# Performance work log

Measured on AMD Instinct MI355X. Metric: run time of the kernel, lower is better.

The kernel has to match this reference:

```python
import jax, jax.numpy as jnp
import numpy as np
import math

B, S, D = 4, 2048, 1024
H = 16
HD = D // H  # 64
NEG_INF = -1e9


def setup_inputs() -> dict:
    key = jax.random.key(0)
    k1, k2, k3, k4, k5 = jax.random.split(key, 5)
    x = jax.random.normal(k1, (B, S, D), dtype=jnp.float32)
    # rotary frequencies (theta = 10000), shape (S, HD//2)
    inv_freq = 1.0 / (10000.0 ** (jnp.arange(0, HD, 2, dtype=jnp.float32) / HD))
    t = jnp.arange(S, dtype=jnp.float32)
    freqs = jnp.outer(t, inv_freq)  # (S, HD//2)
    freqs_cos = jnp.cos(freqs)
    freqs_sin = jnp.sin(freqs)
    # causal additive mask (1,1,S,S)
    causal = jnp.tril(jnp.ones((S, S), dtype=bool))
    mask = jnp.where(causal, 0.0, NEG_INF).astype(jnp.float32)[None, None]
    scale = 0.02
    wq = jax.random.normal(k2, (D, D), dtype=jnp.float32) * scale
    wk = jax.random.normal(k3, (D, D), dtype=jnp.float32) * scale
    wv = jax.random.normal(k4, (D, D), dtype=jnp.float32) * scale
    wo = jax.random.normal(k5, (D, D), dtype=jnp.float32) * scale
    return {"x": x, "freqs_cos": freqs_cos, "freqs_sin": freqs_sin,
            "mask": mask, "wq": wq, "wk": wk, "wv": wv, "wo": wo}


def _apply_rotary(t, cos, sin):
    # t: (B,S,H,HD); cos/sin: (S, HD//2) broadcast as (1,S,1,HD//2)
    tr = t.reshape(*t.shape[:-1], HD // 2, 2)
    t0, t1 = tr[..., 0], tr[..., 1]
    c = cos[None, :, None, :]
    s = sin[None, :, None, :]
    o0 = t0 * c - t1 * s
    o1 = t0 * s + t1 * c
    return jnp.stack([o0, o1], axis=-1).reshape(t.shape)


def reference(x, freqs_cos, freqs_sin, mask, wq, wk, wv, wo):
    bsz, seqlen, _ = x.shape
    xq = (x @ wq).reshape(bsz, seqlen, H, HD)
    xk = (x @ wk).reshape(bsz, seqlen, H, HD)
    xv = (x @ wv).reshape(bsz, seqlen, H, HD)
    xq = _apply_rotary(xq, freqs_cos, freqs_sin)
    xk = _apply_rotary(xk, freqs_cos, freqs_sin)
    # (B,H,S,HD)
    xq = xq.transpose(0, 2, 1, 3)
    xk = xk.transpose(0, 2, 1, 3)
    xv = xv.transpose(0, 2, 1, 3)
    scores = jnp.einsum('bhqd,bhkd->bhqk', xq, xk) / math.sqrt(HD)
    scores = scores + mask
    probs = jax.nn.softmax(scores.astype(jnp.float32), axis=-1).astype(xq.dtype)
    # dropout is identity in eval mode
    out = jnp.einsum('bhqk,bhkd->bhqd', probs, xv)
    out = out.transpose(0, 2, 1, 3).reshape(bsz, seqlen, H * HD)
    return out @ wo
```

## Files before the change

### kernel.cpp

```cpp
#include <hip/hip_runtime.h>
#include <stdint.h>

typedef short short8 __attribute__((ext_vector_type(8)));
typedef float f32x4 __attribute__((ext_vector_type(4)));
typedef float f32x16 __attribute__((ext_vector_type(16)));
typedef unsigned int u32x4 __attribute__((ext_vector_type(4)));
typedef float float4e __attribute__((ext_vector_type(4)));
typedef unsigned short u16;

#define BB 4
#define SS 2048
#define DD 1024
#define HH 16
#define MM (BB*SS)

__device__ __forceinline__ u16 f2bf(float f) {
    unsigned u = __float_as_uint(f);
    u += 0x7FFFu + ((u >> 16) & 1u);
    return (u16)(u >> 16);
}
__device__ __forceinline__ float bf2f(u16 h) {
    return __uint_as_float(((unsigned)h) << 16);
}
__device__ __forceinline__ unsigned cvtpk(float a, float b) {
    unsigned r;
    asm("v_cvt_pk_bf16_f32 %0, %1, %2" : "=v"(r) : "v"(a), "v"(b));
    return r;
}
__device__ __forceinline__ void gload16(const void* g, void* l) {
    __builtin_amdgcn_global_load_lds(
        (const __attribute__((address_space(1))) unsigned int*)(uintptr_t)g,
        (__attribute__((address_space(3))) unsigned int*)(unsigned)(uintptr_t)l,
        16, 0, 0);
}
__device__ __forceinline__ bool tens_is_bf(const u16* mref) { return mref[1] == 0xCE6Eu; }

__global__ __launch_bounds__(256) void cvt_x(const void* xin, u16* xb, const u16* mref) {
    bool isbf = tens_is_bf(mref);
    size_t i = (size_t)blockIdx.x * 256 + threadIdx.x;
    if (isbf) {
        ((u32x4*)xb)[i] = ((const u32x4*)xin)[i];
    } else {
        const float4e* src = (const float4e*)xin;
        float4e a = src[2*i], b = src[2*i+1];
        u32x4 o;
        o[0] = (unsigned)f2bf(a[0]) | ((unsigned)f2bf(a[1]) << 16);
        o[1] = (unsigned)f2bf(a[2]) | ((unsigned)f2bf(a[3]) << 16);
        o[2] = (unsigned)f2bf(b[0]) | ((unsigned)f2bf(b[1]) << 16);
        o[3] = (unsigned)f2bf(b[2]) | ((unsigned)f2bf(b[3]) << 16);
        ((u32x4*)xb)[i] = o;
    }
}

__global__ __launch_bounds__(256) void trw(const void* w0, const void* w1, const void* w2, const void* w3,
                                           u16* wt, const u16* mref) {
    bool isbf = tens_is_bf(mref);
    const void* w = (blockIdx.z == 0) ? w0 : (blockIdx.z == 1) ? w1 : (blockIdx.z == 2) ? w2 : w3;
    u16* out = wt + (size_t)blockIdx.z * (DD*DD);
    __shared__ float t[32][33];
    int tx = threadIdx.x & 31, ty = threadIdx.x >> 5;
    int n0 = blockIdx.x * 32, k0 = blockIdx.y * 32;
#pragma unroll
    for (int i = 0; i < 4; ++i) {
        int k = k0 + ty*4 + i;
        float v = isbf ? bf2f(((const u16*)w)[(size_t)k*DD + n0 + tx])
                       : ((const float*)w)[(size_t)k*DD + n0 + tx];
        t[ty*4 + i][tx] = v;
    }
    __syncthreads();
#pragma unroll
    for (int i = 0; i < 4; ++i)
        out[(size_t)(n0 + ty*4 + i)*DD + k0 + tx] = f2bf(t[tx][ty*4 + i]);
}

template<int MODE>
__global__ __launch_bounds__(256) void gemm128(const u16* __restrict__ A, const u16* __restrict__ Bt,
                                               void* Cout, const void* fcos, const void* fsin,
                                               const u16* mref, float oscale) {
    constexpr int SMEMB = (MODE == 2) ? 36864 : 32768;
    __shared__ __align__(16) unsigned char smem[SMEMB];
    int tid = threadIdx.x;
    int w = tid >> 6, l = tid & 63, lo = l & 15, hi = l >> 4;
    int wm = w >> 1, wn = w & 1;
    int m0 = blockIdx.x * 128, n0 = blockIdx.y * 128;

    f32x4 acc[4][4] = {};

    auto stage = [&](int buf, int t) {
        int k0 = t * 32;
#pragma unroll
        for (int i = 0; i < 2; ++i) {
            int o = (i*256 + tid) * 16;
            int row = o >> 6, inb = o & 63;
            int sw  = inb ^ ((row & 3) << 4);
            gload16((const char*)A + ((size_t)(m0 + row)*DD + k0)*2 + sw,
                    smem + buf*16384 + (i*256 + (tid & ~63))*16);
            gload16((const char*)Bt + ((size_t)(n0 + row)*DD + k0)*2 + sw,
                    smem + buf*16384 + 8192 + (i*256 + (tid & ~63))*16);
        }
    };

    stage(0, 0);
    __syncthreads();
    int cur = 0;
    const int NT = DD / 32;
    for (int t = 0; t < NT; ++t) {
        if (t + 1 < NT) stage(cur ^ 1, t + 1);
        const char* Ab = (const char*)(smem + cur*16384);
        const char* Bb = Ab + 8192;
        short8 af[4], bfr[4];
#pragma unroll
        for (int mi = 0; mi < 4; ++mi) {
            int r = wm*64 + mi*16 + lo;
            int ib = hi * 16;
            af[mi] = *(const short8*)(Ab + r*64 + (ib ^ ((r & 3) << 4)));
        }
#pragma unroll
        for (int ni = 0; ni < 4; ++ni) {
            int r = wn*64 + ni*16 + lo;
            int ib = hi * 16;
            bfr[ni] = *(const short8*)(Bb + r*64 + (ib ^ ((r & 3) << 4)));
        }
        __builtin_amdgcn_s_setprio(1);
#pragma unroll
        for (int mi = 0; mi < 4; ++mi)
#pragma unroll
            for (int ni = 0; ni < 4; ++ni)
                acc[mi][ni] = __builtin_amdgcn_mfma_f32_16x16x32_bf16(af[mi], bfr[ni], acc[mi][ni], 0, 0, 0);
        __builtin_amdgcn_s_setprio(0);
        __syncthreads();
        cur ^= 1;
    }

    if (MODE == 0) {
        bool fbf = (((const u16*)fcos)[0] == 0x3F80u);
        u16* outp = (u16*)Cout;
#pragma unroll
        for (int mi = 0; mi < 4; ++mi)
#pragma unroll
            for (int ni = 0; ni < 4; ++ni)
#pragma unroll
                for (int r = 0; r < 4; ++r) {
                    int gm = m0 + wm*64 + mi*16 + hi*4 + r;
                    int gc = n0 + wn*64 + ni*16 + lo;
                    float v  = acc[mi][ni][r];
                    float vp = __shfl_xor(v, 1);
                    int s = gm & (SS-1), d = gc & 63, i2 = d >> 1;
                    float c, sn;
                    if (fbf) { c = bf2f(((const u16*)fcos)[s*32 + i2]); sn = bf2f(((const u16*)fsin)[s*32 + i2]); }
                    else     { c = ((const float*)fcos)[s*32 + i2];     sn = ((const float*)fsin)[s*32 + i2]; }
                    float o = (gc & 1) ? (vp*sn + v*c) : (v*c - vp*sn);
                    o *= oscale;
                    int b = gm >> 11, h = gc >> 6;
                    outp[((((size_t)b*HH + h)*SS + s) << 6) + d] = f2bf(o);
                }
    } else if (MODE == 2) {
        __syncthreads();
        u16* vs = (u16*)smem + w * (64*72);
#pragma unroll
        for (int ni = 0; ni < 4; ++ni) {
            int d = ni*16 + lo;
#pragma unroll
            for (int mi = 0; mi < 4; ++mi)
#pragma unroll
                for (int rr = 0; rr < 2; ++rr) {
                    unsigned pk = (unsigned)f2bf(acc[mi][ni][2*rr]) | ((unsigned)f2bf(acc[mi][ni][2*rr+1]) << 16);
                    *(unsigned*)(vs + d*72 + mi*16 + hi*4 + rr*2) = pk;
                }
        }
        asm volatile("s_waitcnt lgkmcnt(0)" ::: "memory");
        int bq = (m0 + wm*64) >> 11;
        int s_base = (m0 + wm*64) & (SS-1);
        int h = (n0 + wn*64) >> 6;
        u16* outp = (u16*)Cout;
#pragma unroll
        for (int p = 0; p < 8; ++p) {
            int idx = p*64 + l;
            int row = idx >> 3, ch = idx & 7;
            short8 vv = *(const short8*)(vs + row*72 + ch*8);
            *(short8*)(outp + (((size_t)bq*HH + h)*64 + row)*SS + s_base + ch*8) = vv;
        }
    } else {
        bool isbf = tens_is_bf(mref);
#pragma unroll
        for (int mi = 0; mi < 4; ++mi)
#pragma unroll
            for (int ni = 0; ni < 4; ++ni)
#pragma unroll
                for (int r = 0; r < 4; ++r) {
                    int gm = m0 + wm*64 + mi*16 + hi*4 + r;
                    int gc = n0 + wn*64 + ni*16 + lo;
                    float v = acc[mi][ni][r];
                    if (isbf) ((u16*)Cout)[(size_t)gm*DD + gc] = f2bf(v);
                    else      ((float*)Cout)[(size_t)gm*DD + gc] = v;
                }
    }
}

__global__ __launch_bounds__(256) void attn(const u16* __restrict__ Q, const u16* __restrict__ K,
                                            const u16* __restrict__ VT, u16* __restrict__ AO) {
    __shared__ __align__(16) u16 Kl[2][64*64];
    __shared__ __align__(16) u16 Vl[2][64*64];
    int bh = blockIdx.x;
    int qt = (gridDim.y - 1) - blockIdx.y;
    int tid = threadIdx.x, w = tid >> 6, l = tid & 63;
    int l31 = l & 31, hi5 = l >> 5;
    const u16* Qb = Q  + (size_t)bh * SS * 64;
    const u16* Kb = K  + (size_t)bh * SS * 64;
    const u16* Vb = VT + (size_t)bh * 64 * SS;
    int q0w = qt*128 + w*32;
    int q   = q0w + l31;

    short8 qf[4];
#pragma unroll
    for (int kc = 0; kc < 4; ++kc)
        qf[kc] = *(const short8*)(Qb + (size_t)q*64 + kc*16 + hi5*8);

    f32x16 oacc[2] = {};
    float m_ = -1e30f, l_ = 0.f;

    auto stage = [&](int buf, int kt) {
        const char* Kt = (const char*)(Kb + (size_t)kt*64*64);
        const char* Vt = (const char*)Vb + (size_t)kt*128;
#pragma unroll
        for (int i = 0; i < 2; ++i) {
            int idx = i*256 + tid;
            int row = idx >> 3, inb = (idx & 7) * 16;
            int sw = inb ^ ((row & 7) << 4);
            gload16(Kt + row*128 + sw,            (char*)Kl[buf] + (i*256 + (tid & ~63))*16);
            gload16(Vt + (size_t)row*(SS*2) + sw, (char*)Vl[buf] + (i*256 + (tid & ~63))*16);
        }
    };

    int nkt = 2*qt + 2;
    stage(0, 0);
    __syncthreads();
    int cur = 0;

    for (int kt = 0; kt < nkt; ++kt) {
        if (kt + 1 < nkt) stage(cur ^ 1, kt + 1);

        if (kt*64 <= q0w + 31) {
            f32x16 sc[2] = {};
            __builtin_amdgcn_s_setprio(1);
#pragma unroll
            for (int kvt = 0; kvt < 2; ++kvt) {
                short8 kf[4];
#pragma unroll
                for (int kc = 0; kc < 4; ++kc) {
                    int row = kvt*32 + l31;
                    int ib = kc*32 + hi5*16;
                    kf[kc] = *(const short8*)((const char*)Kl[cur] + row*128 + (ib ^ ((row & 7) << 4)));
                }
#pragma unroll
                for (int kc = 0; kc < 4; ++kc)
                    sc[kvt] = __builtin_amdgcn_mfma_f32_32x32x16_bf16(kf[kc], qf[kc], sc[kvt], 0, 0, 0);
            }
            __builtin_amdgcn_s_setprio(0);

            if (kt*64 + 63 > q0w) {
#pragma unroll
                for (int kvt = 0; kvt < 2; ++kvt)
#pragma unroll
                    for (int rg = 0; rg < 16; ++rg) {
                        int kv = kt*64 + kvt*32 + (rg & 3) + 8*(rg >> 2) + 4*hi5;
                        if (kv > q) sc[kvt][rg] = -1e9f;
                    }
            }

            float mx = -1e30f;
#pragma unroll
            for (int kvt = 0; kvt < 2; ++kvt)
#pragma unroll
                for (int rg = 0; rg < 16; ++rg) mx = fmaxf(mx, sc[kvt][rg]);
            mx = fmaxf(mx, __shfl_xor(mx, 32));
            float mn = fmaxf(m_, mx);
            float al = __expf(m_ - mn);
            float rs = 0.f;
#pragma unroll
            for (int kvt = 0; kvt < 2; ++kvt)
#pragma unroll
                for (int rg = 0; rg < 16; ++rg) {
                    float p = __expf(sc[kvt][rg] - mn);
                    sc[kvt][rg] = p;
                    rs += p;
                }
            rs += __shfl_xor(rs, 32);
            m_ = mn;
            l_ = l_ * al + rs;
#pragma unroll
            for (int dt = 0; dt < 2; ++dt)
#pragma unroll
                for (int rg = 0; rg < 16; ++rg) oacc[dt][rg] *= al;

            short8 pa[4];
#pragma unroll
            for (int kc = 0; kc < 4; ++kc) {
                const int kvt = kc >> 1;
                const int base = (kc & 1) * 8;
                unsigned A0 = cvtpk(sc[kvt][base + 0], sc[kvt][base + 1]);
                unsigned A1 = cvtpk(sc[kvt][base + 2], sc[kvt][base + 3]);
                unsigned B0 = cvtpk(sc[kvt][base + 4], sc[kvt][base + 5]);
                unsigned B1 = cvtpk(sc[kvt][base + 6], sc[kvt][base + 7]);
                asm("v_permlane32_swap_b32 %0, %1" : "+v"(A0), "+v"(B0));
                asm("v_permlane32_swap_b32 %0, %1" : "+v"(A1), "+v"(B1));
                u32x4 pk; pk[0] = A0; pk[1] = A1; pk[2] = B0; pk[3] = B1;
                pa[kc] = __builtin_bit_cast(short8, pk);
            }

            __builtin_amdgcn_s_setprio(1);
#pragma unroll
            for (int dt = 0; dt < 2; ++dt) {
                short8 vf[4];
#pragma unroll
                for (int kc = 0; kc < 4; ++kc) {
                    int row = dt*32 + l31;
                    int ib = kc*32 + hi5*16;
                    vf[kc] = *(const short8*)((const char*)Vl[cur] + row*128 + (ib ^ ((row & 7) << 4)));
                }
#pragma unroll
                for (int kc = 0; kc < 4; ++kc)
                    oacc[dt] = __builtin_amdgcn_mfma_f32_32x32x16_bf16(vf[kc], pa[kc], oacc[dt], 0, 0, 0);
            }
            __builtin_amdgcn_s_setprio(0);
        }

        __syncthreads();
        cur ^= 1;
    }

    int b = bh >> 4, h = bh & 15;
    float inv = 1.0f / l_;
    u16* aor = AO + (size_t)(b*SS + q)*DD + h*64;
#pragma unroll
    for (int dt = 0; dt < 2; ++dt)
#pragma unroll
        for (int j = 0; j < 8; ++j) {
            int r0 = 2*j, r1 = 2*j + 1;
            int d = dt*32 + (r0 & 3) + 8*(r0 >> 2) + 4*hi5;
            unsigned pk = (unsigned)f2bf(oacc[dt][r0] * inv) | ((unsigned)f2bf(oacc[dt][r1] * inv) << 16);
            *(unsigned*)(aor + d) = pk;
        }
}

extern "C" void kernel_launch(void* const* d_in, const int* in_sizes, int n_in,
                              void* d_out, int out_size, void* d_ws, size_t ws_size,
                              hipStream_t stream) {
    const void* x    = d_in[0];
    const void* fcos = d_in[1];
    const void* fsin = d_in[2];
    const u16*  mref = (const u16*)d_in[3];
    const void* wq   = d_in[4];
    const void* wk   = d_in[5];
    const void* wv   = d_in[6];
    const void* wo   = d_in[7];

    u16* ws = (u16*)d_ws;
    const size_t XB = (size_t)MM * DD;
    const size_t WT = (size_t)DD * DD;
    u16* xb  = ws;
    u16* wt  = ws + XB;
    u16* qb  = ws + XB + 4*WT;
    u16* kb  = qb + XB;
    u16* vtb = kb + XB;

    cvt_x<<<4096, 256, 0, stream>>>(x, xb, mref);
    trw<<<dim3(32, 32, 4), 256, 0, stream>>>(wq, wk, wv, wo, wt, mref);
    gemm128<0><<<dim3(64, 8), 256, 0, stream>>>(xb, wt,        qb,  fcos, fsin, mref, 0.125f);
    gemm128<0><<<dim3(64, 8), 256, 0, stream>>>(xb, wt + WT,   kb,  fcos, fsin, mref, 1.0f);
    gemm128<2><<<dim3(64, 8), 256, 0, stream>>>(xb, wt + 2*WT, vtb, fcos, fsin, mref, 1.0f);
    attn<<<dim3(64, 16), 256, 0, stream>>>(qb, kb, vtb, xb);
    gemm128<3><<<dim3(64, 8), 256, 0, stream>>>(xb, wt + 3*WT, d_out, fcos, fsin, mref, 1.0f);
}
```

Baseline: 194.8 us.

## Fuse QKV projections into one launch, add grid swizzle and lazy softmax rescale

The three Q/K/V projection GEMMs now run as a single 1536-block launch over the concatenated transposed weights, and each tile picks the Q, K or V-transpose epilogue from its column range. Block indices are remapped so groups of consecutive workgroups share weight tiles, which should improve L2 reuse. In attention, the Q scale now folds in log2(e) so the softmax can use exp2f, and the running-max rescale of the accumulators is skipped unless the new max exceeds the old one by more than 8. The intent is to cut launch overhead, tail effects and softmax VALU work. The lazy rescale lets unnormalised exponentials reach up to 2^8, which assumes fp32 and bf16 headroom is enough.

```diff
diff --git a/kernel.cpp b/kernel.cpp
--- a/kernel.cpp
+++ b/kernel.cpp
@@ -73,16 +73,22 @@
         out[(size_t)(n0 + ty*4 + i)*DD + k0 + tx] = f2bf(t[tx][ty*4 + i]);
 }
 
+#define QSCALE 0.1803368801111204f
 template<int MODE>
 __global__ __launch_bounds__(256) void gemm128(const u16* __restrict__ A, const u16* __restrict__ Bt,
-                                               void* Cout, const void* fcos, const void* fsin,
-                                               const u16* mref, float oscale) {
-    constexpr int SMEMB = (MODE == 2) ? 36864 : 32768;
+                                               u16* outQ, u16* outK, u16* outVT, void* Cout,
+                                               const void* fcos, const void* fsin,
+                                               const u16* mref) {
+    constexpr int SMEMB = (MODE == 1) ? 36864 : 32768;
     __shared__ __align__(16) unsigned char smem[SMEMB];
     int tid = threadIdx.x;
     int w = tid >> 6, l = tid & 63, lo = l & 15, hi = l >> 4;
     int wm = w >> 1, wn = w & 1;
-    int m0 = blockIdx.x * 128, n0 = blockIdx.y * 128;
+    int wg = blockIdx.x;
+    int c = wg & 7, local = wg >> 3;
+    int bx = c*8 + (local & 7);
+    int by = local >> 3;
+    int m0 = bx * 128, n0 = by * 128;
 
     f32x4 acc[4][4] = {};
 
@@ -132,53 +138,57 @@
         cur ^= 1;
     }
 
-    if (MODE == 0) {
-        bool fbf = (((const u16*)fcos)[0] == 0x3F80u);
-        u16* outp = (u16*)Cout;
-#pragma unroll
-        for (int mi = 0; mi < 4; ++mi)
-#pragma unroll
-            for (int ni = 0; ni < 4; ++ni)
-#pragma unroll
-                for (int r = 0; r < 4; ++r) {
-                    int gm = m0 + wm*64 + mi*16 + hi*4 + r;
-                    int gc = n0 + wn*64 + ni*16 + lo;
-                    float v  = acc[mi][ni][r];
-                    float vp = __shfl_xor(v, 1);
-                    int s = gm & (SS-1), d = gc & 63, i2 = d >> 1;
-                    float c, sn;
-                    if (fbf) { c = bf2f(((const u16*)fcos)[s*32 + i2]); sn = bf2f(((const u16*)fsin)[s*32 + i2]); }
-                    else     { c = ((const float*)fcos)[s*32 + i2];     sn = ((const float*)fsin)[s*32 + i2]; }
-                    float o = (gc & 1) ? (vp*sn + v*c) : (v*c - vp*sn);
-                    o *= oscale;
-                    int b = gm >> 11, h = gc >> 6;
-                    outp[((((size_t)b*HH + h)*SS + s) << 6) + d] = f2bf(o);
-                }
-    } else if (MODE == 2) {
-        __syncthreads();
-        u16* vs = (u16*)smem + w * (64*72);
-#pragma unroll
-        for (int ni = 0; ni < 4; ++ni) {
-            int d = ni*16 + lo;
+    if (MODE == 1) {
+        int wi = n0 >> 10;
+        int n0w = n0 & 1023;
+        if (wi == 2) {
+            __syncthreads();
+            u16* vs = (u16*)smem + w * (64*72);
+#pragma unroll
+            for (int ni = 0; ni < 4; ++ni) {
+                int d = ni*16 + lo;
+#pragma unroll
+                for (int mi = 0; mi < 4; ++mi)
+#pragma unroll
+                    for (int rr = 0; rr < 2; ++rr) {
+                        unsigned pk = (unsigned)f2bf(acc[mi][ni][2*rr]) | ((unsigned)f2bf(acc[mi][ni][2*rr+1]) << 16);
+                        *(unsigned*)(vs + d*72 + mi*16 + hi*4 + rr*2) = pk;
+                    }
+            }
+            asm volatile("s_waitcnt lgkmcnt(0)" ::: "memory");
+            int bq = (m0 + wm*64) >> 11;
+            int s_base = (m0 + wm*64) & (SS-1);
+            int h = (n0w + wn*64) >> 6;
+#pragma unroll
+            for (int p = 0; p < 8; ++p) {
+                int idx = p*64 + l;
+                int row = idx >> 3, ch = idx & 7;
+                short8 vv = *(const short8*)(vs + row*72 + ch*8);
+                *(short8*)(outVT + (((size_t)bq*HH + h)*64 + row)*SS + s_base + ch*8) = vv;
+            }
+        } else {
+            bool fbf = (((const u16*)fcos)[0] == 0x3F80u);
+            u16* outp = wi ? outK : outQ;
+            float oscale = wi ? 1.0f : QSCALE;
 #pragma unroll
             for (int mi = 0; mi < 4; ++mi)
 #pragma unroll
-                for (int rr = 0; rr < 2; ++rr) {
-                    unsigned pk = (unsigned)f2bf(acc[mi][ni][2*rr]) | ((unsigned)f2bf(acc[mi][ni][2*rr+1]) << 16);
-                    *(unsigned*)(vs + d*72 + mi*16 + hi*4 + rr*2) = pk;
-                }
-        }
-        asm volatile("s_waitcnt lgkmcnt(0)" ::: "memory");
-        int bq = (m0 + wm*64) >> 11;
-        int s_base = (m0 + wm*64) & (SS-1);
-        int h = (n0 + wn*64) >> 6;
-        u16* outp = (u16*)Cout;
-#pragma unroll
-        for (int p = 0; p < 8; ++p) {
-            int idx = p*64 + l;
-            int row = idx >> 3, ch = idx & 7;
-            short8 vv = *(const short8*)(vs + row*72 + ch*8);
-            *(short8*)(outp + (((size_t)bq*HH + h)*64 + row)*SS + s_base + ch*8) = vv;
+                for (int ni = 0; ni < 4; ++ni)
+#pragma unroll
+                    for (int r = 0; r < 4; ++r) {
+                        int gm = m0 + wm*64 + mi*16 + hi*4 + r;
+                        int gc = n0w + wn*64 + ni*16 + lo;
+                        float v  = acc[mi][ni][r];
+                        float vp = __shfl_xor(v, 1);
+                        int s = gm & (SS-1), d = gc & 63, i2 = d >> 1;
+                        float co, sn;
+                        if (fbf) { co = bf2f(((const u16*)fcos)[s*32 + i2]); sn = bf2f(((const u16*)fsin)[s*32 + i2]); }
+                        else     { co = ((const float*)fcos)[s*32 + i2];     sn = ((const float*)fsin)[s*32 + i2]; }
+                        float o = (gc & 1) ? (vp*sn + v*co) : (v*co - vp*sn);
+                        o *= oscale;
+                        int b = gm >> 11, h = gc >> 6;
+                        outp[((((size_t)b*HH + h)*SS + s) << 6) + d] = f2bf(o);
+                    }
         }
     } else {
         bool isbf = tens_is_bf(mref);
@@ -274,24 +284,27 @@
 #pragma unroll
                 for (int rg = 0; rg < 16; ++rg) mx = fmaxf(mx, sc[kvt][rg]);
             mx = fmaxf(mx, __shfl_xor(mx, 32));
-            float mn = fmaxf(m_, mx);
-            float al = __expf(m_ - mn);
+            if (!__all(mx <= m_ + 8.f)) {
+                float mn = fmaxf(m_, mx);
+                float al = exp2f(m_ - mn);
+                m_ = mn;
+                l_ *= al;
+#pragma unroll
+                for (int dt = 0; dt < 2; ++dt)
+#pragma unroll
+                    for (int rg = 0; rg < 16; ++rg) oacc[dt][rg] *= al;
+            }
             float rs = 0.f;
 #pragma unroll
             for (int kvt = 0; kvt < 2; ++kvt)
 #pragma unroll
                 for (int rg = 0; rg < 16; ++rg) {
-                    float p = __expf(sc[kvt][rg] - mn);
+                    float p = exp2f(sc[kvt][rg] - m_);
                     sc[kvt][rg] = p;
                     rs += p;
                 }
             rs += __shfl_xor(rs, 32);
-            m_ = mn;
-            l_ = l_ * al + rs;
-#pragma unroll
-            for (int dt = 0; dt < 2; ++dt)
-#pragma unroll
-                for (int rg = 0; rg < 16; ++rg) oacc[dt][rg] *= al;
+            l_ += rs;
 
             short8 pa[4];
 #pragma unroll
@@ -366,9 +379,7 @@
 
     cvt_x<<<4096, 256, 0, stream>>>(x, xb, mref);
     trw<<<dim3(32, 32, 4), 256, 0, stream>>>(wq, wk, wv, wo, wt, mref);
-    gemm128<0><<<dim3(64, 8), 256, 0, stream>>>(xb, wt,        qb,  fcos, fsin, mref, 0.125f);
-    gemm128<0><<<dim3(64, 8), 256, 0, stream>>>(xb, wt + WT,   kb,  fcos, fsin, mref, 1.0f);
-    gemm128<2><<<dim3(64, 8), 256, 0, stream>>>(xb, wt + 2*WT, vtb, fcos, fsin, mref, 1.0f);
+    gemm128<1><<<1536, 256, 0, stream>>>(xb, wt, qb, kb, vtb, nullptr, fcos, fsin, mref);
     attn<<<dim3(64, 16), 256, 0, stream>>>(qb, kb, vtb, xb);
-    gemm128<3><<<dim3(64, 8), 256, 0, stream>>>(xb, wt + 3*WT, d_out, fcos, fsin, mref, 1.0f);
-}
+    gemm128<3><<<512, 256, 0, stream>>>(xb, wt + 3*WT, nullptr, nullptr, nullptr, d_out, fcos, fsin, mref);
+}
```

New measurement: 200.5 us. 2.9% more time.

## Triple-buffer attention K/V loads and use exp2 softmax with lazy rescaling

Applied to the files above, without the earlier changes.

The attention kernel moves from double to triple buffering of the K/V LDS tiles. It prefetches two tiles ahead and replaces __syncthreads with explicit vmcnt waits plus a raw barrier. Softmax now works in base 2: log2(e)/sqrt(d) is folded into the Q scale, __expf becomes exp2f, and the running-max rescale of the output accumulator only happens when the new max exceeds the old one by more than 8. Swizzled LDS offsets are hoisted out of the loop, and the max and sum reductions are tree-structured. The cost is more LDS per block, which may reduce occupancy, and the vmcnt counting must stay correct.

```diff
diff --git a/kernel.cpp b/kernel.cpp
--- a/kernel.cpp
+++ b/kernel.cpp
@@ -34,6 +34,7 @@
         16, 0, 0);
 }
 __device__ __forceinline__ bool tens_is_bf(const u16* mref) { return mref[1] == 0xCE6Eu; }
+#define PIPE_BAR() do { __builtin_amdgcn_sched_barrier(0); __builtin_amdgcn_s_barrier(); __builtin_amdgcn_sched_barrier(0); } while(0)
 
 __global__ __launch_bounds__(256) void cvt_x(const void* xin, u16* xb, const u16* mref) {
     bool isbf = tens_is_bf(mref);
@@ -73,6 +74,7 @@
         out[(size_t)(n0 + ty*4 + i)*DD + k0 + tx] = f2bf(t[tx][ty*4 + i]);
 }
 
+#define QSCALE 0.1803368801111204f
 template<int MODE>
 __global__ __launch_bounds__(256) void gemm128(const u16* __restrict__ A, const u16* __restrict__ Bt,
                                                void* Cout, const void* fcos, const void* fsin,
@@ -146,10 +148,10 @@
                     float v  = acc[mi][ni][r];
                     float vp = __shfl_xor(v, 1);
                     int s = gm & (SS-1), d = gc & 63, i2 = d >> 1;
-                    float c, sn;
-                    if (fbf) { c = bf2f(((const u16*)fcos)[s*32 + i2]); sn = bf2f(((const u16*)fsin)[s*32 + i2]); }
-                    else     { c = ((const float*)fcos)[s*32 + i2];     sn = ((const float*)fsin)[s*32 + i2]; }
-                    float o = (gc & 1) ? (vp*sn + v*c) : (v*c - vp*sn);
+                    float co, sn;
+                    if (fbf) { co = bf2f(((const u16*)fcos)[s*32 + i2]); sn = bf2f(((const u16*)fsin)[s*32 + i2]); }
+                    else     { co = ((const float*)fcos)[s*32 + i2];     sn = ((const float*)fsin)[s*32 + i2]; }
+                    float o = (gc & 1) ? (vp*sn + v*co) : (v*co - vp*sn);
                     o *= oscale;
                     int b = gm >> 11, h = gc >> 6;
                     outp[((((size_t)b*HH + h)*SS + s) << 6) + d] = f2bf(o);
@@ -199,8 +201,8 @@
 
 __global__ __launch_bounds__(256) void attn(const u16* __restrict__ Q, const u16* __restrict__ K,
                                             const u16* __restrict__ VT, u16* __restrict__ AO) {
-    __shared__ __align__(16) u16 Kl[2][64*64];
-    __shared__ __align__(16) u16 Vl[2][64*64];
+    __shared__ __align__(16) u16 Kl[3][64*64];
+    __shared__ __align__(16) u16 Vl[3][64*64];
     int bh = blockIdx.x;
     int qt = (gridDim.y - 1) - blockIdx.y;
     int tid = threadIdx.x, w = tid >> 6, l = tid & 63;
@@ -216,6 +218,16 @@
     for (int kc = 0; kc < 4; ++kc)
         qf[kc] = *(const short8*)(Qb + (size_t)q*64 + kc*16 + hi5*8);
 
+    int loff[2][4];
+#pragma unroll
+    for (int g = 0; g < 2; ++g)
+#pragma unroll
+        for (int kc = 0; kc < 4; ++kc) {
+            int row = g*32 + l31;
+            int ib = kc*32 + hi5*16;
+            loff[g][kc] = row*128 + (ib ^ ((row & 7) << 4));
+        }
+
     f32x16 oacc[2] = {};
     float m_ = -1e30f, l_ = 0.f;
 
@@ -234,24 +246,27 @@
 
     int nkt = 2*qt + 2;
     stage(0, 0);
-    __syncthreads();
+    stage(1, 1);
+    asm volatile("s_waitcnt vmcnt(4)" ::: "memory");
+    PIPE_BAR();
+
     int cur = 0;
-
     for (int kt = 0; kt < nkt; ++kt) {
-        if (kt + 1 < nkt) stage(cur ^ 1, kt + 1);
+        int nx = cur + 2; if (nx >= 3) nx -= 3;
+        bool pre = (kt + 2 < nkt);
+        if (pre) stage(nx, kt + 2);
 
         if (kt*64 <= q0w + 31) {
+            const char* Kc = (const char*)Kl[cur];
+            const char* Vc = (const char*)Vl[cur];
             f32x16 sc[2] = {};
             __builtin_amdgcn_s_setprio(1);
 #pragma unroll
             for (int kvt = 0; kvt < 2; ++kvt) {
                 short8 kf[4];
 #pragma unroll
-                for (int kc = 0; kc < 4; ++kc) {
-                    int row = kvt*32 + l31;
-                    int ib = kc*32 + hi5*16;
-                    kf[kc] = *(const short8*)((const char*)Kl[cur] + row*128 + (ib ^ ((row & 7) << 4)));
-                }
+                for (int kc = 0; kc < 4; ++kc)
+                    kf[kc] = *(const short8*)(Kc + loff[kvt][kc]);
 #pragma unroll
                 for (int kc = 0; kc < 4; ++kc)
                     sc[kvt] = __builtin_amdgcn_mfma_f32_32x32x16_bf16(kf[kc], qf[kc], sc[kvt], 0, 0, 0);
@@ -268,30 +283,35 @@
                     }
             }
 
-            float mx = -1e30f;
+            float m8[8];
+#pragma unroll
+            for (int j = 0; j < 8; ++j)
+                m8[j] = fmaxf(fmaxf(sc[0][j], sc[0][j+8]), fmaxf(sc[1][j], sc[1][j+8]));
+            float mx = fmaxf(fmaxf(fmaxf(m8[0], m8[1]), fmaxf(m8[2], m8[3])),
+                             fmaxf(fmaxf(m8[4], m8[5]), fmaxf(m8[6], m8[7])));
+            mx = fmaxf(mx, __shfl_xor(mx, 32));
+            if (!__all(mx <= m_ + 8.f)) {
+                float mn = fmaxf(m_, mx);
+                float al = exp2f(m_ - mn);
+                m_ = mn;
+                l_ *= al;
+#pragma unroll
+                for (int dt = 0; dt < 2; ++dt)
+#pragma unroll
+                    for (int rg = 0; rg < 16; ++rg) oacc[dt][rg] *= al;
+            }
 #pragma unroll
             for (int kvt = 0; kvt < 2; ++kvt)
 #pragma unroll
-                for (int rg = 0; rg < 16; ++rg) mx = fmaxf(mx, sc[kvt][rg]);
-            mx = fmaxf(mx, __shfl_xor(mx, 32));
-            float mn = fmaxf(m_, mx);
-            float al = __expf(m_ - mn);
-            float rs = 0.f;
-#pragma unroll
-            for (int kvt = 0; kvt < 2; ++kvt)
-#pragma unroll
-                for (int rg = 0; rg < 16; ++rg) {
-                    float p = __expf(sc[kvt][rg] - mn);
-                    sc[kvt][rg] = p;
-                    rs += p;
-                }
+                for (int rg = 0; rg < 16; ++rg)
+                    sc[kvt][rg] = exp2f(sc[kvt][rg] - m_);
+            float s8[8];
+#pragma unroll
+            for (int j = 0; j < 8; ++j)
+                s8[j] = (sc[0][j] + sc[0][j+8]) + (sc[1][j] + sc[1][j+8]);
+            float rs = ((s8[0] + s8[1]) + (s8[2] + s8[3])) + ((s8[4] + s8[5]) + (s8[6] + s8[7]));
             rs += __shfl_xor(rs, 32);
-            m_ = mn;
-            l_ = l_ * al + rs;
-#pragma unroll
-            for (int dt = 0; dt < 2; ++dt)
-#pragma unroll
-                for (int rg = 0; rg < 16; ++rg) oacc[dt][rg] *= al;
+            l_ += rs;
 
             short8 pa[4];
 #pragma unroll
@@ -313,11 +333,8 @@
             for (int dt = 0; dt < 2; ++dt) {
                 short8 vf[4];
 #pragma unroll
-                for (int kc = 0; kc < 4; ++kc) {
-                    int row = dt*32 + l31;
-                    int ib = kc*32 + hi5*16;
-                    vf[kc] = *(const short8*)((const char*)Vl[cur] + row*128 + (ib ^ ((row & 7) << 4)));
-                }
+                for (int kc = 0; kc < 4; ++kc)
+                    vf[kc] = *(const short8*)(Vc + loff[dt][kc]);
 #pragma unroll
                 for (int kc = 0; kc < 4; ++kc)
                     oacc[dt] = __builtin_amdgcn_mfma_f32_32x32x16_bf16(vf[kc], pa[kc], oacc[dt], 0, 0, 0);
@@ -325,8 +342,10 @@
             __builtin_amdgcn_s_setprio(0);
         }
 
-        __syncthreads();
-        cur ^= 1;
+        if (pre) asm volatile("s_waitcnt vmcnt(4)" ::: "memory");
+        else     asm volatile("s_waitcnt vmcnt(0)" ::: "memory");
+        PIPE_BAR();
+        cur = (cur == 2) ? 0 : cur + 1;
     }
 
     int b = bh >> 4, h = bh & 15;
@@ -366,7 +385,7 @@
 
     cvt_x<<<4096, 256, 0, stream>>>(x, xb, mref);
     trw<<<dim3(32, 32, 4), 256, 0, stream>>>(wq, wk, wv, wo, wt, mref);
-    gemm128<0><<<dim3(64, 8), 256, 0, stream>>>(xb, wt,        qb,  fcos, fsin, mref, 0.125f);
+    gemm128<0><<<dim3(64, 8), 256, 0, stream>>>(xb, wt,        qb,  fcos, fsin, mref, QSCALE);
     gemm128<0><<<dim3(64, 8), 256, 0, stream>>>(xb, wt + WT,   kb,  fcos, fsin, mref, 1.0f);
     gemm128<2><<<dim3(64, 8), 256, 0, stream>>>(xb, wt + 2*WT, vtb, fcos, fsin, mref, 1.0f);
     attn<<<dim3(64, 16), 256, 0, stream>>>(qb, kb, vtb, xb);
```

After: 206.5 us. 1.06x slower.

## Widen attention KV tile to 128 and fold log2e into Q scale for exp2

Applied to the files above, without the earlier changes.

The attention kernel now stages 128-key K/V tiles per iteration instead of 64, which halves the number of loop iterations, barriers and softmax rescale steps. Masking is applied only on the diagonal tile, and the per-wave skip of fully masked tiles is removed. The Q scale now includes log2(e), so the softmax uses exp2f directly. In exchange the kernel uses twice the shared memory and more registers, which may lower occupancy, and waves near the diagonal do some wasted work on masked keys.

```diff
diff --git a/kernel.cpp b/kernel.cpp
--- a/kernel.cpp
+++ b/kernel.cpp
@@ -73,6 +73,7 @@
         out[(size_t)(n0 + ty*4 + i)*DD + k0 + tx] = f2bf(t[tx][ty*4 + i]);
 }
 
+#define QSCALE 0.1803368801111204f
 template<int MODE>
 __global__ __launch_bounds__(256) void gemm128(const u16* __restrict__ A, const u16* __restrict__ Bt,
                                                void* Cout, const void* fcos, const void* fsin,
@@ -112,14 +113,12 @@
 #pragma unroll
         for (int mi = 0; mi < 4; ++mi) {
             int r = wm*64 + mi*16 + lo;
-            int ib = hi * 16;
-            af[mi] = *(const short8*)(Ab + r*64 + (ib ^ ((r & 3) << 4)));
+            af[mi] = *(const short8*)(Ab + r*64 + ((hi*16) ^ ((r & 3) << 4)));
         }
 #pragma unroll
         for (int ni = 0; ni < 4; ++ni) {
             int r = wn*64 + ni*16 + lo;
-            int ib = hi * 16;
-            bfr[ni] = *(const short8*)(Bb + r*64 + (ib ^ ((r & 3) << 4)));
+            bfr[ni] = *(const short8*)(Bb + r*64 + ((hi*16) ^ ((r & 3) << 4)));
         }
         __builtin_amdgcn_s_setprio(1);
 #pragma unroll
@@ -146,10 +145,10 @@
                     float v  = acc[mi][ni][r];
                     float vp = __shfl_xor(v, 1);
                     int s = gm & (SS-1), d = gc & 63, i2 = d >> 1;
-                    float c, sn;
-                    if (fbf) { c = bf2f(((const u16*)fcos)[s*32 + i2]); sn = bf2f(((const u16*)fsin)[s*32 + i2]); }
-                    else     { c = ((const float*)fcos)[s*32 + i2];     sn = ((const float*)fsin)[s*32 + i2]; }
-                    float o = (gc & 1) ? (vp*sn + v*c) : (v*c - vp*sn);
+                    float co, sn;
+                    if (fbf) { co = bf2f(((const u16*)fcos)[s*32 + i2]); sn = bf2f(((const u16*)fsin)[s*32 + i2]); }
+                    else     { co = ((const float*)fcos)[s*32 + i2];     sn = ((const float*)fsin)[s*32 + i2]; }
+                    float o = (gc & 1) ? (vp*sn + v*co) : (v*co - vp*sn);
                     o *= oscale;
                     int b = gm >> 11, h = gc >> 6;
                     outp[((((size_t)b*HH + h)*SS + s) << 6) + d] = f2bf(o);
@@ -199,8 +198,8 @@
 
 __global__ __launch_bounds__(256) void attn(const u16* __restrict__ Q, const u16* __restrict__ K,
                                             const u16* __restrict__ VT, u16* __restrict__ AO) {
-    __shared__ __align__(16) u16 Kl[2][64*64];
-    __shared__ __align__(16) u16 Vl[2][64*64];
+    __shared__ __align__(16) u16 Kl[2][128*64];
+    __shared__ __align__(16) u16 Vl[2][64*128];
     int bh = blockIdx.x;
     int qt = (gridDim.y - 1) - blockIdx.y;
     int tid = threadIdx.x, w = tid >> 6, l = tid & 63;
@@ -208,8 +207,7 @@
     const u16* Qb = Q  + (size_t)bh * SS * 64;
     const u16* Kb = K  + (size_t)bh * SS * 64;
     const u16* Vb = VT + (size_t)bh * 64 * SS;
-    int q0w = qt*128 + w*32;
-    int q   = q0w + l31;
+    int q = qt*128 + w*32 + l31;
 
     short8 qf[4];
 #pragma unroll
@@ -220,19 +218,25 @@
     float m_ = -1e30f, l_ = 0.f;
 
     auto stage = [&](int buf, int kt) {
-        const char* Kt = (const char*)(Kb + (size_t)kt*64*64);
-        const char* Vt = (const char*)Vb + (size_t)kt*128;
-#pragma unroll
-        for (int i = 0; i < 2; ++i) {
+        const char* Kt = (const char*)Kb + (size_t)kt*(128*128);
+        const char* Vt = (const char*)Vb + (size_t)kt*256;
+#pragma unroll
+        for (int i = 0; i < 4; ++i) {
             int idx = i*256 + tid;
-            int row = idx >> 3, inb = (idx & 7) * 16;
-            int sw = inb ^ ((row & 7) << 4);
-            gload16(Kt + row*128 + sw,            (char*)Kl[buf] + (i*256 + (tid & ~63))*16);
-            gload16(Vt + (size_t)row*(SS*2) + sw, (char*)Vl[buf] + (i*256 + (tid & ~63))*16);
+            {
+                int row = idx >> 3, inb = (idx & 7) * 16;
+                int sw = inb ^ ((row & 7) << 4);
+                gload16(Kt + (size_t)row*128 + sw, (char*)Kl[buf] + (i*256 + (tid & ~63))*16);
+            }
+            {
+                int row = idx >> 4, inb = (idx & 15) * 16;
+                int sw = inb ^ ((row & 7) << 4);
+                gload16(Vt + (size_t)row*(SS*2) + sw, (char*)Vl[buf] + (i*256 + (tid & ~63))*16);
+            }
         }
     };
 
-    int nkt = 2*qt + 2;
+    int nkt = qt + 1;
     stage(0, 0);
     __syncthreads();
     int cur = 0;
@@ -240,90 +244,89 @@
     for (int kt = 0; kt < nkt; ++kt) {
         if (kt + 1 < nkt) stage(cur ^ 1, kt + 1);
 
-        if (kt*64 <= q0w + 31) {
-            f32x16 sc[2] = {};
-            __builtin_amdgcn_s_setprio(1);
-#pragma unroll
-            for (int kvt = 0; kvt < 2; ++kvt) {
-                short8 kf[4];
-#pragma unroll
-                for (int kc = 0; kc < 4; ++kc) {
-                    int row = kvt*32 + l31;
-                    int ib = kc*32 + hi5*16;
-                    kf[kc] = *(const short8*)((const char*)Kl[cur] + row*128 + (ib ^ ((row & 7) << 4)));
+        const char* Kc = (const char*)Kl[cur];
+        const char* Vc = (const char*)Vl[cur];
+
+        f32x16 sc[4];
+#pragma unroll
+        for (int kvt = 0; kvt < 4; ++kvt) sc[kvt] = (f32x16)0.f;
+        __builtin_amdgcn_s_setprio(1);
+#pragma unroll
+        for (int kvt = 0; kvt < 4; ++kvt) {
+            int row = kvt*32 + l31;
+            short8 kf[4];
+#pragma unroll
+            for (int kc = 0; kc < 4; ++kc)
+                kf[kc] = *(const short8*)(Kc + row*128 + ((kc*32 + hi5*16) ^ ((row & 7) << 4)));
+#pragma unroll
+            for (int kc = 0; kc < 4; ++kc)
+                sc[kvt] = __builtin_amdgcn_mfma_f32_32x32x16_bf16(kf[kc], qf[kc], sc[kvt], 0, 0, 0);
+        }
+        __builtin_amdgcn_s_setprio(0);
+
+        if (kt == qt) {
+#pragma unroll
+            for (int kvt = 0; kvt < 4; ++kvt)
+#pragma unroll
+                for (int rg = 0; rg < 16; ++rg) {
+                    int kv = kt*128 + kvt*32 + (rg & 3) + 8*(rg >> 2) + 4*hi5;
+                    if (kv > q) sc[kvt][rg] = -1e9f;
                 }
-#pragma unroll
-                for (int kc = 0; kc < 4; ++kc)
-                    sc[kvt] = __builtin_amdgcn_mfma_f32_32x32x16_bf16(kf[kc], qf[kc], sc[kvt], 0, 0, 0);
+        }
+
+        float mx = -1e30f;
+#pragma unroll
+        for (int kvt = 0; kvt < 4; ++kvt)
+#pragma unroll
+            for (int rg = 0; rg < 16; ++rg) mx = fmaxf(mx, sc[kvt][rg]);
+        mx = fmaxf(mx, __shfl_xor(mx, 32));
+        float mn = fmaxf(m_, mx);
+        float al = exp2f(m_ - mn);
+        float rs = 0.f;
+#pragma unroll
+        for (int kvt = 0; kvt < 4; ++kvt)
+#pragma unroll
+            for (int rg = 0; rg < 16; ++rg) {
+                float p = exp2f(sc[kvt][rg] - mn);
+                sc[kvt][rg] = p;
+                rs += p;
             }
-            __builtin_amdgcn_s_setprio(0);
-
-            if (kt*64 + 63 > q0w) {
-#pragma unroll
-                for (int kvt = 0; kvt < 2; ++kvt)
-#pragma unroll
-                    for (int rg = 0; rg < 16; ++rg) {
-                        int kv = kt*64 + kvt*32 + (rg & 3) + 8*(rg >> 2) + 4*hi5;
-                        if (kv > q) sc[kvt][rg] = -1e9f;
-                    }
-            }
-
-            float mx = -1e30f;
-#pragma unroll
-            for (int kvt = 0; kvt < 2; ++kvt)
-#pragma unroll
-                for (int rg = 0; rg < 16; ++rg) mx = fmaxf(mx, sc[kvt][rg]);
-            mx = fmaxf(mx, __shfl_xor(mx, 32));
-            float mn = fmaxf(m_, mx);
-            float al = __expf(m_ - mn);
-            float rs = 0.f;
-#pragma unroll
-            for (int kvt = 0; kvt < 2; ++kvt)
-#pragma unroll
-                for (int rg = 0; rg < 16; ++rg) {
-                    float p = __expf(sc[kvt][rg] - mn);
-                    sc[kvt][rg] = p;
-                    rs += p;
-                }
-            rs += __shfl_xor(rs, 32);
-            m_ = mn;
-            l_ = l_ * al + rs;
-#pragma unroll
-            for (int dt = 0; dt < 2; ++dt)
-#pragma unroll
-                for (int rg = 0; rg < 16; ++rg) oacc[dt][rg] *= al;
-
-            short8 pa[4];
-#pragma unroll
-            for (int kc = 0; kc < 4; ++kc) {
-                const int kvt = kc >> 1;
-                const int base = (kc & 1) * 8;
-                unsigned A0 = cvtpk(sc[kvt][base + 0], sc[kvt][base + 1]);
-                unsigned A1 = cvtpk(sc[kvt][base + 2], sc[kvt][base + 3]);
-                unsigned B0 = cvtpk(sc[kvt][base + 4], sc[kvt][base + 5]);
-                unsigned B1 = cvtpk(sc[kvt][base + 6], sc[kvt][base + 7]);
-                asm("v_permlane32_swap_b32 %0, %1" : "+v"(A0), "+v"(B0));
-                asm("v_permlane32_swap_b32 %0, %1" : "+v"(A1), "+v"(B1));
-                u32x4 pk; pk[0] = A0; pk[1] = A1; pk[2] = B0; pk[3] = B1;
-                pa[kc] = __builtin_bit_cast(short8, pk);
-            }
-
-            __builtin_amdgcn_s_setprio(1);
-#pragma unroll
-            for (int dt = 0; dt < 2; ++dt) {
-                short8 vf[4];
-#pragma unroll
-                for (int kc = 0; kc < 4; ++kc) {
-                    int row = dt*32 + l31;
-                    int ib = kc*32 + hi5*16;
-                    vf[kc] = *(const short8*)((const char*)Vl[cur] + row*128 + (ib ^ ((row & 7) << 4)));
-                }
-#pragma unroll
-                for (int kc = 0; kc < 4; ++kc)
-                    oacc[dt] = __builtin_amdgcn_mfma_f32_32x32x16_bf16(vf[kc], pa[kc], oacc[dt], 0, 0, 0);
-            }
-            __builtin_amdgcn_s_setprio(0);
-        }
+        rs += __shfl_xor(rs, 32);
+        m_ = mn;
+        l_ = l_ * al + rs;
+#pragma unroll
+        for (int dt = 0; dt < 2; ++dt)
+#pragma unroll
+            for (int rg = 0; rg < 16; ++rg) oacc[dt][rg] *= al;
+
+        short8 pa[8];
+#pragma unroll
+        for (int kc = 0; kc < 8; ++kc) {
+            const int kvt = kc >> 1;
+            const int base = (kc & 1) * 8;
+            unsigned A0 = cvtpk(sc[kvt][base + 0], sc[kvt][base + 1]);
+            unsigned A1 = cvtpk(sc[kvt][base + 2], sc[kvt][base + 3]);
+            unsigned B0 = cvtpk(sc[kvt][base + 4], sc[kvt][base + 5]);
+            unsigned B1 = cvtpk(sc[kvt][base + 6], sc[kvt][base + 7]);
+            asm("v_permlane32_swap_b32 %0, %1" : "+v"(A0), "+v"(B0));
+            asm("v_permlane32_swap_b32 %0, %1" : "+v"(A1), "+v"(B1));
+            u32x4 pk; pk[0] = A0; pk[1] = A1; pk[2] = B0; pk[3] = B1;
+            pa[kc] = __builtin_bit_cast(short8, pk);
+        }
+
+        __builtin_amdgcn_s_setprio(1);
+#pragma unroll
+        for (int dt = 0; dt < 2; ++dt) {
+            int row = dt*32 + l31;
+            short8 vf[8];
+#pragma unroll
+            for (int kc = 0; kc < 8; ++kc)
+                vf[kc] = *(const short8*)(Vc + row*256 + ((kc*32 + hi5*16) ^ ((row & 7) << 4)));
+#pragma unroll
+            for (int kc = 0; kc < 8; ++kc)
+                oacc[dt] = __builtin_amdgcn_mfma_f32_32x32x16_bf16(vf[kc], pa[kc], oacc[dt], 0, 0, 0);
+        }
+        __builtin_amdgcn_s_setprio(0);
 
         __syncthreads();
         cur ^= 1;
@@ -366,7 +369,7 @@
 
     cvt_x<<<4096, 256, 0, stream>>>(x, xb, mref);
     trw<<<dim3(32, 32, 4), 256, 0, stream>>>(wq, wk, wv, wo, wt, mref);
-    gemm128<0><<<dim3(64, 8), 256, 0, stream>>>(xb, wt,        qb,  fcos, fsin, mref, 0.125f);
+    gemm128<0><<<dim3(64, 8), 256, 0, stream>>>(xb, wt,        qb,  fcos, fsin, mref, QSCALE);
     gemm128<0><<<dim3(64, 8), 256, 0, stream>>>(xb, wt + WT,   kb,  fcos, fsin, mref, 1.0f);
     gemm128<2><<<dim3(64, 8), 256, 0, stream>>>(xb, wt + 2*WT, vtb, fcos, fsin, mref, 1.0f);
     attn<<<dim3(64, 16), 256, 0, stream>>>(qb, kb, vtb, xb);
```

After: 230.0 us. +18.0%, slower.
